# Kernel tuning notes

Measured on AMD Instinct MI355X. Metric: run time of the kernel, lower is better.

## Reference

```python
import jax, jax.numpy as jnp
import numpy as np

Z, K, HID = 128, 256, 512  # z_size, key_size, hidden_size


def setup_inputs() -> dict:
    key = jax.random.key(0)
    ks = jax.random.split(key, 12)
    B, T, Hi, Wi, Y = 512, 32, 32, 32, 4
    D = Hi * Wi
    s = 0.02
    f32 = jnp.float32
    return {
        "x_seq": jax.random.normal(ks[0], (B, T, Hi, Wi), f32),
        "W_enc": jax.random.normal(ks[1], (D, Z), f32) * s,
        "b_enc": jnp.zeros((Z,), f32),
        "W_lstm": jax.random.normal(ks[2], (K + 1, 4 * HID), f32) * s,
        "U_lstm": jax.random.normal(ks[3], (HID, 4 * HID), f32) * s,
        "b_lstm": jnp.zeros((4 * HID,), f32),
        "W_key": jax.random.normal(ks[4], (HID, K), f32) * s,
        "b_key": jnp.zeros((K,), f32),
        "W_g": jax.random.normal(ks[5], (HID, 1), f32) * s,
        "b_g": jnp.zeros((1,), f32),
        "W_y": jax.random.normal(ks[6], (HID, Y), f32) * s,
        "b_y": jnp.zeros((Y,), f32),
        "gamma": jnp.ones((Z,), f32),
        "beta": jnp.zeros((Z,), f32),
        "conf_gain": jnp.float32(1.0),
        "conf_bias": jnp.float32(0.0),
    }


def _forward(x_seq, W_enc, b_enc, W_lstm, U_lstm, b_lstm, W_key, b_key,
             W_g, b_g, W_y, b_y, gamma, beta, conf_gain, conf_bias):
    B, T = x_seq.shape[0], x_seq.shape[1]
    N = T + 1  # memory slots after final null step
    x = x_seq.reshape(B, T, -1)
    z = jax.nn.relu(x @ W_enc + b_enc)  # (B,T,Z) encoder stand-in
    # Faithful to TF source: list of (B,Z) stacks to (T,B,Z) and reduce axis 1
    # -> normalization is over the BATCH axis.
    mu = jnp.mean(z, axis=0, keepdims=True)
    var = jnp.var(z, axis=0, keepdims=True)
    z = (z - mu) / jnp.sqrt(var + 1e-8) * gamma + beta
    z_full = jnp.concatenate([z, jnp.zeros((B, 1, Z), z.dtype)], axis=1)  # (B,N,Z)

    def lstm_cell(x_in, h_in, c_in):
        gates = x_in @ W_lstm + h_in @ U_lstm + b_lstm
        i, f, g_, o = jnp.split(gates, 4, axis=-1)  # keras gate order i,f,c,o
        c_new = jax.nn.sigmoid(f) * c_in + jax.nn.sigmoid(i) * jnp.tanh(g_)
        h_new = jax.nn.sigmoid(o) * jnp.tanh(c_new)
        return h_new, c_new

    slot_ids = jnp.arange(N)

    def step(carry, inp):
        h, c, key_r, M_k, M_v = carry
        z_t, t = inp  # z_t: (B,Z), t: scalar step index
        # Faithful: source passes initial_state=(cell_state, hidden), swapping roles.
        h_new, c_new = lstm_cell(key_r, c, h)
        key_w = jax.nn.relu(h_new @ W_key + b_key)          # (B,K)
        g = jax.nn.sigmoid(h_new @ W_g + b_g)               # (B,1)
        y_lin = jax.nn.softmax(h_new @ W_y + b_y, axis=-1)  # (B,Y)
        # content-addressable read over the t filled slots
        sim = jnp.einsum('bz,bnz->bn', z_t, M_v)            # (B,N)
        mask = (slot_ids < t)[None, :]
        w_k = jax.nn.softmax(jnp.where(mask, sim, -1e9), axis=1)
        c_k = jax.nn.sigmoid(sim * conf_gain + conf_bias)   # (B,N)
        mem = jnp.concatenate([M_k, c_k[..., None]], axis=2)  # (B,N,K+1)
        weighted = jnp.einsum('bn,bnp->bp', w_k, mem)       # (B,K+1)
        key_r_new = jnp.where(t == 0, jnp.zeros_like(key_r), g * weighted)
        # write into slot t (pre-allocated memory, masked read above)
        M_k = M_k.at[:, t, :].set(key_w)
        M_v = M_v.at[:, t, :].set(z_t)
        return (h_new, c_new, key_r_new, M_k, M_v), y_lin

    h0 = jnp.zeros((B, HID), z.dtype)
    c0 = jnp.zeros((B, HID), z.dtype)
    kr0 = jnp.zeros((B, K + 1), z.dtype)
    Mk0 = jnp.zeros((B, N, K), z.dtype)
    Mv0 = jnp.zeros((B, N, Z), z.dtype)
    xs = (jnp.swapaxes(z_full, 0, 1), slot_ids)
    _, ys = jax.lax.scan(step, (h0, c0, kr0, Mk0, Mv0), xs)
    return ys[-1]  # y_pred_linear from the final (null-input) step


def reference(x_seq, W_enc, b_enc, W_lstm, U_lstm, b_lstm, W_key, b_key,
              W_g, b_g, W_y, b_y, gamma, beta, conf_gain, conf_bias):
    return _forward(x_seq, W_enc, b_enc, W_lstm, U_lstm, b_lstm, W_key, b_key,
                    W_g, b_g, W_y, b_y, gamma, beta, conf_gain, conf_bias)
```

## Files before the change

kernel.cpp:

```cpp
#include <hip/hip_runtime.h>

typedef __attribute__((ext_vector_type(8))) short short8;
typedef __attribute__((ext_vector_type(4))) float f32x4;
typedef __attribute__((ext_vector_type(8))) unsigned short ushort8;
typedef __attribute__((ext_vector_type(4))) unsigned short ushort4v;

__device__ __forceinline__ unsigned short f2bf(float f) {
  union { float f; unsigned u; } v; v.f = f;
  unsigned u = v.u;
  u += 0x7fffu + ((u >> 16) & 1u);
  return (unsigned short)(u >> 16);
}
__device__ __forceinline__ float sigm(float x) { return 1.f / (1.f + __expf(-x)); }
__device__ __forceinline__ float ftanh(float x) { return 1.f - 2.f / (__expf(2.f * x) + 1.f); }

__device__ __forceinline__ void gl16(const unsigned short* g, unsigned short* l) {
  __builtin_amdgcn_global_load_lds((const __attribute__((address_space(1))) void*)g,
                                   (__attribute__((address_space(3))) void*)l, 16, 0, 0);
}

__device__ __forceinline__ uint4 ld16_sys(const void* base, int off) {
  uint4 r;
  asm volatile("global_load_dwordx4 %0, %1, %2 sc0 sc1"
               : "=v"(r) : "v"(off), "s"(base) : "memory");
  return r;
}
__device__ __forceinline__ uint4 ld16_asm(const void* base, int off) {
  uint4 r;
  asm volatile("global_load_dwordx4 %0, %1, %2"
               : "=v"(r) : "v"(off), "s"(base) : "memory");
  return r;
}
__device__ __forceinline__ float ldf_sys(const void* base, int off) {
  float r;
  asm volatile("global_load_dword %0, %1, %2 sc0 sc1"
               : "=v"(r) : "v"(off), "s"(base) : "memory");
  return r;
}
__device__ __forceinline__ void stf_sys(void* base, int off, float v) {
  asm volatile("global_store_dword %0, %1, %2 sc0 sc1"
               :: "v"(off), "v"(v), "s"(base) : "memory");
}
__device__ __forceinline__ void sth_sys(void* base, int off, unsigned short v) {
  asm volatile("global_store_short %0, %1, %2 sc0 sc1"
               :: "v"(off), "v"(v), "s"(base) : "memory");
}
#define WAITVM(N)                                          \
  asm volatile("s_waitcnt vmcnt(" #N ")" ::: "memory");    \
  __builtin_amdgcn_sched_barrier(0)

__device__ __forceinline__ void gbar(unsigned* cnt, unsigned* gen) {
  asm volatile("s_waitcnt vmcnt(0)" ::: "memory");
  __syncthreads();
  if (threadIdx.x == 0) {
    unsigned g = __hip_atomic_load(gen, __ATOMIC_RELAXED, __HIP_MEMORY_SCOPE_AGENT);
    unsigned a = __hip_atomic_fetch_add(cnt, 1u, __ATOMIC_RELAXED, __HIP_MEMORY_SCOPE_AGENT);
    if (a == 255u) {
      __hip_atomic_store(cnt, 0u, __ATOMIC_RELAXED, __HIP_MEMORY_SCOPE_AGENT);
      __hip_atomic_store(gen, g + 1u, __ATOMIC_RELAXED, __HIP_MEMORY_SCOPE_AGENT);
    } else {
      while (__hip_atomic_load(gen, __ATOMIC_RELAXED, __HIP_MEMORY_SCOPE_AGENT) == g)
        __builtin_amdgcn_s_sleep(2);
    }
  }
  __syncthreads();
}

#define LSTR 40

__global__ void k_prep(const float* __restrict__ W_lstm, const float* __restrict__ U_lstm,
                       const float* __restrict__ W_enc, const float* __restrict__ W_key,
                       const float* __restrict__ W_g, const float* __restrict__ W_y,
                       const float* __restrict__ b_key, const float* __restrict__ b_g,
                       const float* __restrict__ b_y,
                       unsigned short* __restrict__ WcombT, unsigned short* __restrict__ Wk2T,
                       unsigned short* __restrict__ WencT, float* __restrict__ bias2,
                       unsigned short* __restrict__ xinA, unsigned short* __restrict__ xinB,
                       float* __restrict__ h, float* __restrict__ z_full,
                       unsigned* __restrict__ bar) {
  const int N1 = 2048 * 800, N2 = 320 * 512, N3 = 128 * 1024, N4 = 320,
            N5 = 512 * 800, N7 = 512 * 512, N8 = 512 * 128, N9 = 256;
  int i = blockIdx.x * 256 + threadIdx.x;
  if (i < N1) {
    int np = i / 800, k = i - np * 800;
    int j = np >> 2, gate = np & 3, n = gate * 512 + j;
    float v = 0.f;
    if (k < 257) v = W_lstm[k * 2048 + n];
    else if (k >= 288) v = U_lstm[(k - 288) * 2048 + n];
    WcombT[i] = f2bf(v);
    return;
  }
  i -= N1;
  if (i < N2) {
    int n = i / 512, k = i - n * 512;
    float v = 0.f;
    if (n < 256) v = W_key[k * 256 + n];
    else if (n == 256) v = W_g[k];
    else if (n < 261) v = W_y[k * 4 + (n - 257)];
    Wk2T[i] = f2bf(v);
    return;
  }
  i -= N2;
  if (i < N3) {
    int n = i / 1024, k = i - n * 1024;
    WencT[i] = f2bf(W_enc[k * 128 + n]);
    return;
  }
  i -= N3;
  if (i < N4) {
    float v = (i < 256) ? b_key[i] : (i == 256 ? b_g[0] : (i < 261 ? b_y[i - 257] : 0.f));
    bias2[i] = v;
    return;
  }
  i -= N4;
  if (i < N5) { xinA[i] = 0; return; }
  i -= N5;
  if (i < N5) { xinB[i] = 0; return; }
  i -= N5;
  if (i < N7) { h[i] = 0.f; return; }
  i -= N7;
  if (i < N8) {
    int b = i >> 7, z = i & 127;
    z_full[(b * 33 + 32) * 128 + z] = 0.f;
    return;
  }
  i -= N8;
  if (i < N9) bar[i] = 0;
}

__global__ __launch_bounds__(512) void k_enc(const float* __restrict__ x,
                                             const unsigned short* __restrict__ WencT,
                                             const float* __restrict__ b_enc,
                                             float* __restrict__ zbuf) {
  __shared__ __align__(16) unsigned short As[2][64 * LSTR];
  __shared__ __align__(16) unsigned short Bs[2][128 * LSTR];
  int tid = threadIdx.x;
  int m0 = blockIdx.x * 64;
  int lane = tid & 63, wid = tid >> 6;
  int wm = (wid >> 2) * 32, wn = (wid & 3) * 32;
  int q = lane >> 4, r = lane & 15;
  int ldrowA = tid >> 3, ldcA = (tid & 7) * 4;
  int ldrowB = tid >> 2, ldcB = (tid & 3) * 8;
  const float4* Ag = reinterpret_cast<const float4*>(x + (size_t)(m0 + ldrowA) * 1024);
  const uint4* Bg = reinterpret_cast<const uint4*>(WencT + (size_t)ldrowB * 1024);
  float4 ra = Ag[ldcA >> 2];
  uint4 rb = Bg[ldcB >> 3];
  f32x4 acc[2][2] = {};
  int s = 0;
  {
    ushort4v t4;
    t4[0] = f2bf(ra.x); t4[1] = f2bf(ra.y); t4[2] = f2bf(ra.z); t4[3] = f2bf(ra.w);
    *reinterpret_cast<ushort4v*>(&As[0][ldrowA * LSTR + ldcA]) = t4;
    *reinterpret_cast<uint4*>(&Bs[0][ldrowB * LSTR + ldcB]) = rb;
  }
  __syncthreads();
  for (int kk = 0; kk < 32; ++kk) {
    if (kk < 31) {
      int k0 = (kk + 1) * 32;
      ra = Ag[(k0 + ldcA) >> 2];
      rb = Bg[(k0 + ldcB) >> 3];
    }
    short8 a0 = *reinterpret_cast<const short8*>(&As[s][(wm + r) * LSTR + q * 8]);
    short8 a1 = *reinterpret_cast<const short8*>(&As[s][(wm + 16 + r) * LSTR + q * 8]);
    short8 b0 = *reinterpret_cast<const short8*>(&Bs[s][(wn + r) * LSTR + q * 8]);
    short8 b1 = *reinterpret_cast<const short8*>(&Bs[s][(wn + 16 + r) * LSTR + q * 8]);
    acc[0][0] = __builtin_amdgcn_mfma_f32_16x16x32_bf16(a0, b0, acc[0][0], 0, 0, 0);
    acc[0][1] = __builtin_amdgcn_mfma_f32_16x16x32_bf16(a0, b1, acc[0][1], 0, 0, 0);
    acc[1][0] = __builtin_amdgcn_mfma_f32_16x16x32_bf16(a1, b0, acc[1][0], 0, 0, 0);
    acc[1][1] = __builtin_amdgcn_mfma_f32_16x16x32_bf16(a1, b1, acc[1][1], 0, 0, 0);
    if (kk < 31) {
      ushort4v t4;
      t4[0] = f2bf(ra.x); t4[1] = f2bf(ra.y); t4[2] = f2bf(ra.z); t4[3] = f2bf(ra.w);
      *reinterpret_cast<ushort4v*>(&As[s ^ 1][ldrowA * LSTR + ldcA]) = t4;
      *reinterpret_cast<uint4*>(&Bs[s ^ 1][ldrowB * LSTR + ldcB]) = rb;
      s ^= 1;
    }
    __syncthreads();
  }
#pragma unroll
  for (int mt = 0; mt < 2; ++mt)
#pragma unroll
    for (int nt = 0; nt < 2; ++nt)
#pragma unroll
      for (int e = 0; e < 4; ++e) {
        int row = m0 + wm + mt * 16 + q * 4 + e;
        int col = wn + nt * 16 + r;
        zbuf[(size_t)row * 128 + col] = fmaxf(acc[mt][nt][e] + b_enc[col], 0.f);
      }
}

__global__ __launch_bounds__(256) void k_ln(const float* __restrict__ zbuf,
                                            const float* __restrict__ gamma,
                                            const float* __restrict__ beta,
                                            float* __restrict__ z_full) {
  int bid = blockIdx.x;
  int tstep = bid >> 3;
  int z0 = (bid & 7) * 16;
  int tid = threadIdx.x;
  int zl = tid & 15, bg = tid >> 4;
  __shared__ float ps[256], qs[256];
  __shared__ float muS[16], rsS[16];
  float s = 0.f, ss = 0.f;
  for (int ii = 0; ii < 32; ++ii) {
    int b = bg * 32 + ii;
    float v = zbuf[(size_t)(b * 32 + tstep) * 128 + z0 + zl];
    s += v; ss += v * v;
  }
  ps[tid] = s; qs[tid] = ss;
  __syncthreads();
  if (tid < 16) {
    float S = 0.f, Q = 0.f;
    for (int g2 = 0; g2 < 16; ++g2) { S += ps[g2 * 16 + tid]; Q += qs[g2 * 16 + tid]; }
    float mu = S / 512.f;
    float var = Q / 512.f - mu * mu;
    muS[tid] = mu;
    rsS[tid] = rsqrtf(var + 1e-8f);
  }
  __syncthreads();
  float ga = gamma[z0 + zl], be = beta[z0 + zl];
  float mu = muS[zl], rs = rsS[zl];
  for (int ii = 0; ii < 32; ++ii) {
    int b = bg * 32 + ii;
    float v = zbuf[(size_t)(b * 32 + tstep) * 128 + z0 + zl];
    z_full[(size_t)(b * 33 + tstep) * 128 + z0 + zl] = (v - mu) * rs * ga + be;
  }
}

__global__ __launch_bounds__(256) void k_attnpre(const float* __restrict__ z_full,
                                                 const float* __restrict__ cgain,
                                                 const float* __restrict__ cbias,
                                                 float* __restrict__ wk_tbl,
                                                 float* __restrict__ wck_tbl) {
  __shared__ float zs[33 * 128];
  __shared__ float sim[33 * 33];
  int b = blockIdx.x, tid = threadIdx.x;
  const float* zb = z_full + (size_t)b * 33 * 128;
  for (int i = tid; i < 33 * 128; i += 256) zs[i] = zb[i];
  __syncthreads();
  for (int p = tid; p < 33 * 33; p += 256) {
    int t = p / 33, n = p - t * 33;
    float s = 0.f;
    if (n < t) {
#pragma unroll 8
      for (int k2 = 0; k2 < 128; ++k2) s += zs[t * 128 + k2] * zs[n * 128 + k2];
    }
    sim[p] = s;
  }
  __syncthreads();
  if (tid >= 1 && tid < 33) {
    int t = tid;
    float cg = cgain[0], cb2 = cbias[0];
    float m = -3.0e38f;
    for (int n = 0; n < t; ++n) m = fmaxf(m, sim[t * 33 + n]);
    float ssum = 0.f;
    for (int n = 0; n < t; ++n) ssum += __expf(sim[t * 33 + n] - m);
    float inv = 1.f / ssum;
    float wck = 0.f;
    for (int n = 0; n < t; ++n) {
      float wk = __expf(sim[t * 33 + n] - m) * inv;
      wk_tbl[((size_t)b * 33 + t) * 33 + n] = wk;
      float ck = 1.f / (1.f + __expf(-(sim[t * 33 + n] * cg + cb2)));
      wck += wk * ck;
    }
    wck_tbl[b * 33 + t] = wck;
  }
}

__global__ __launch_bounds__(256) void k_loop(
    unsigned short* __restrict__ xinA, unsigned short* __restrict__ xinB,
    const unsigned short* __restrict__ WT, const float* __restrict__ b_lstm,
    float* __restrict__ h, unsigned short* __restrict__ hbf,
    const unsigned short* __restrict__ Wk2T, const float* __restrict__ bias2,
    float* __restrict__ Mk, float* __restrict__ logits,
    const float* __restrict__ Wg, const float* __restrict__ bg,
    const float* __restrict__ wk_tbl, const float* __restrict__ wck_tbl,
    float* __restrict__ out, unsigned* __restrict__ bar) {
  __shared__ __align__(16) unsigned short Bres[64 * 808];
  __shared__ __align__(16) unsigned char scr[43136];
  unsigned* cnt = bar;
  unsigned* gen = bar + 64;
  const int tid = threadIdx.x, bid = blockIdx.x;
  const int lane = tid & 63, w = tid >> 6;
  const int q = lane >> 4, r = lane & 15;
  const int wm = (w >> 1) * 32, wn = (w & 1) * 32;
  const int nn = bid & 31, mi = bid >> 5;
  const int m0 = mi * 64, n0g = nn * 64;

  for (int l = 0; l < 26; ++l) {
    int gw = l * 256 + w * 64;
    if (gw < 6464) {
      int g = gw + lane;
      int row = g / 101, cg = g - row * 101;
      int col = (cg >= 100) ? 792 : cg * 8;
      gl16(WT + (size_t)(n0g + row) * 800 + col, Bres + gw * 8);
    }
  }

  int srow[5], scol[5];
#pragma unroll
  for (int l = 0; l < 5; ++l) {
    int idx = l * 256 + tid;
    srow[l] = idx / 20;
    scol[l] = (idx - srow[l] * 20) * 8;
  }
  unsigned short* A0 = (unsigned short*)scr;
  unsigned short* A1 = (unsigned short*)(scr + 21504);

  const int jl = tid & 15, jg = nn * 16 + jl, rl0 = tid >> 4;
  const float bL0 = b_lstm[jg], bL1 = b_lstm[512 + jg],
              bL2 = b_lstm[1024 + jg], bL3 = b_lstm[1536 + jg];
  float hreg[4] = {0.f, 0.f, 0.f, 0.f};

  const int mi2 = bid / 5, ni2 = bid - mi2 * 5;

  asm volatile("s_waitcnt vmcnt(0)" ::: "memory");
  __syncthreads();

  for (int t = 0; t < 33; ++t) {
    const unsigned short* cur = (t & 1) ? xinB : xinA;
    unsigned short* nxt = (t & 1) ? xinA : xinB;

    uint4 R[5];
#pragma unroll
    for (int l = 0; l < 5; ++l)
      R[l] = ld16_sys(cur, ((m0 + srow[l]) * 800 + scol[l]) * 2);
    asm volatile("s_waitcnt vmcnt(0)" ::: "memory");
    __builtin_amdgcn_sched_barrier(0);
#pragma unroll
    for (int l = 0; l < 5; ++l)
      *(uint4*)&A0[srow[l] * 168 + scol[l]] = R[l];
    __syncthreads();

    f32x4 acc[2][2] = {};
    for (int c = 0; c < 5; ++c) {
      const unsigned short* Ac = (c & 1) ? A1 : A0;
      unsigned short* An = (c & 1) ? A0 : A1;
      if (c < 4) {
#pragma unroll
        for (int l = 0; l < 5; ++l)
          R[l] = ld16_sys(cur, ((m0 + srow[l]) * 800 + (c + 1) * 160 + scol[l]) * 2);
      }
#pragma unroll
      for (int ks = 0; ks < 5; ++ks) {
        short8 a0 = *(const short8*)&Ac[(wm + r) * 168 + ks * 32 + q * 8];
        short8 a1 = *(const short8*)&Ac[(wm + 16 + r) * 168 + ks * 32 + q * 8];
        short8 b0 = *(const short8*)&Bres[(wn + r) * 808 + c * 160 + ks * 32 + q * 8];
        short8 b1 = *(const short8*)&Bres[(wn + 16 + r) * 808 + c * 160 + ks * 32 + q * 8];
        acc[0][0] = __builtin_amdgcn_mfma_f32_16x16x32_bf16(a0, b0, acc[0][0], 0, 0, 0);
        acc[0][1] = __builtin_amdgcn_mfma_f32_16x16x32_bf16(a0, b1, acc[0][1], 0, 0, 0);
        acc[1][0] = __builtin_amdgcn_mfma_f32_16x16x32_bf16(a1, b0, acc[1][0], 0, 0, 0);
        acc[1][1] = __builtin_amdgcn_mfma_f32_16x16x32_bf16(a1, b1, acc[1][1], 0, 0, 0);
      }
      if (c < 4) {
        asm volatile("s_waitcnt vmcnt(0)" ::: "memory");
        __builtin_amdgcn_sched_barrier(0);
#pragma unroll
        for (int l = 0; l < 5; ++l)
          *(uint4*)&An[srow[l] * 168 + scol[l]] = R[l];
        __syncthreads();
      }
    }
    __syncthreads();

    float* Cs = (float*)scr;
#pragma unroll
    for (int mt = 0; mt < 2; ++mt)
#pragma unroll
      for (int nt = 0; nt < 2; ++nt)
#pragma unroll
        for (int e = 0; e < 4; ++e)
          Cs[(wm + mt * 16 + q * 4 + e) * 65 + wn + nt * 16 + r] = acc[mt][nt][e];
    __syncthreads();
#pragma unroll
    for (int it = 0; it < 4; ++it) {
      int rl = it * 16 + rl0;
      int brow = m0 + rl;
      float gi = Cs[rl * 65 + jl * 4 + 0] + bL0;
      float gf = Cs[rl * 65 + jl * 4 + 1] + bL1;
      float gc = Cs[rl * 65 + jl * 4 + 2] + bL2;
      float go = Cs[rl * 65 + jl * 4 + 3] + bL3;
      float cnew = sigm(gf) * hreg[it] + sigm(gi) * ftanh(gc);
      float hnew = sigm(go) * ftanh(cnew);
      hreg[it] = hnew;
      stf_sys(h, (brow * 512 + jg) * 4, hnew);
      sth_sys(hbf, (brow * 512 + jg) * 2, f2bf(hnew));
      sth_sys(nxt, (brow * 800 + 288 + jg) * 2, f2bf(cnew));
    }
    gbar(cnt, gen);

    if (bid < 40) {
      int m0b = mi2 * 64, n0b = ni2 * 64;
      int aoff0 = ((m0b + wm + r) * 512 + q * 8) * 2;
      int aoff1 = aoff0 + 16 * 1024;
      int boff0 = ((n0b + wn + r) * 512 + q * 8) * 2;
      int boff1 = boff0 + 16 * 1024;
      uint4 ab[4][2], bb[4][2];
      f32x4 acc2[2][2] = {};
#pragma unroll
      for (int j = 0; j < 3; ++j) {
        ab[j][0] = ld16_sys(hbf, aoff0 + j * 64);
        ab[j][1] = ld16_sys(hbf, aoff1 + j * 64);
        bb[j][0] = ld16_asm(Wk2T, boff0 + j * 64);
        bb[j][1] = ld16_asm(Wk2T, boff1 + j * 64);
      }
#pragma unroll
      for (int kk = 0; kk < 16; ++kk) {
        if (kk < 13) {
          int j = kk + 3;
          ab[j & 3][0] = ld16_sys(hbf, aoff0 + j * 64);
          ab[j & 3][1] = ld16_sys(hbf, aoff1 + j * 64);
          bb[j & 3][0] = ld16_asm(Wk2T, boff0 + j * 64);
          bb[j & 3][1] = ld16_asm(Wk2T, boff1 + j * 64);
        }
        if (kk < 13) { WAITVM(12); }
        else if (kk == 13) { WAITVM(8); }
        else if (kk == 14) { WAITVM(4); }
        else { WAITVM(0); }
        short8 a0 = *(const short8*)&ab[kk & 3][0];
        short8 a1 = *(const short8*)&ab[kk & 3][1];
        short8 b0s = *(const short8*)&bb[kk & 3][0];
        short8 b1s = *(const short8*)&bb[kk & 3][1];
        acc2[0][0] = __builtin_amdgcn_mfma_f32_16x16x32_bf16(a0, b0s, acc2[0][0], 0, 0, 0);
        acc2[0][1] = __builtin_amdgcn_mfma_f32_16x16x32_bf16(a0, b1s, acc2[0][1], 0, 0, 0);
        acc2[1][0] = __builtin_amdgcn_mfma_f32_16x16x32_bf16(a1, b0s, acc2[1][0], 0, 0, 0);
        acc2[1][1] = __builtin_amdgcn_mfma_f32_16x16x32_bf16(a1, b1s, acc2[1][1], 0, 0, 0);
      }
#pragma unroll
      for (int mt = 0; mt < 2; ++mt)
#pragma unroll
        for (int nt = 0; nt < 2; ++nt)
#pragma unroll
          for (int e2 = 0; e2 < 4; ++e2) {
            int row = m0b + wm + mt * 16 + q * 4 + e2;
            int np = n0b + wn + nt * 16 + r;
            float v = acc2[mt][nt][e2] + bias2[np];
            if (np < 256)
              stf_sys(Mk, ((row * 33 + t) * 256 + np) * 4, fmaxf(v, 0.f));
            else if (np >= 257 && np < 261)
              stf_sys(logits, (row * 4 + (np - 257)) * 4, v);
          }
    } else if (t > 0 && t < 32) {
      float* wkS = (float*)scr;
      float* red4 = (float*)(scr + 512);
      int b0 = bid - 40, b1 = b0 + 216, b2 = b0 + 432;
      bool v2 = (b2 < 512);
      int b2s = v2 ? b2 : b0;
      float hv[3][2];
      hv[0][0] = ldf_sys(h, (b0 * 512 + tid) * 4);
      hv[0][1] = ldf_sys(h, (b0 * 512 + 256 + tid) * 4);
      hv[1][0] = ldf_sys(h, (b1 * 512 + tid) * 4);
      hv[1][1] = ldf_sys(h, (b1 * 512 + 256 + tid) * 4);
      hv[2][0] = ldf_sys(h, (b2s * 512 + tid) * 4);
      hv[2][1] = ldf_sys(h, (b2s * 512 + 256 + tid) * 4);
      asm volatile("s_waitcnt vmcnt(0)" ::: "memory");
      __builtin_amdgcn_sched_barrier(0);
      float wg0 = Wg[tid], wg1 = Wg[256 + tid], bgv = bg[0];
#pragma unroll
      for (int rr = 0; rr < 3; ++rr) {
        int b = (rr == 0) ? b0 : (rr == 1) ? b1 : b2s;
        bool wr = (rr < 2) || v2;
        float sd = hv[rr][0] * wg0 + hv[rr][1] * wg1;
#pragma unroll
        for (int off = 32; off > 0; off >>= 1) sd += __shfl_down(sd, off);
        if (lane == 0) red4[w] = sd;
        if (tid < t) wkS[tid] = wk_tbl[((size_t)b * 33 + t) * 33 + tid];
        __syncthreads();
        float g = 1.f / (1.f + __expf(-(red4[0] + red4[1] + red4[2] + red4[3] + bgv)));
        float p0 = 0.f, p1 = 0.f, p2 = 0.f, p3 = 0.f;
        int n = 0;
        for (; n + 4 <= t; n += 4) {
          p0 += wkS[n] * Mk[((size_t)b * 33 + n) * 256 + tid];
          p1 += wkS[n + 1] * Mk[((size_t)b * 33 + n + 1) * 256 + tid];
          p2 += wkS[n + 2] * Mk[((size_t)b * 33 + n + 2) * 256 + tid];
          p3 += wkS[n + 3] * Mk[((size_t)b * 33 + n + 3) * 256 + tid];
        }
        for (; n < t; ++n) p0 += wkS[n] * Mk[((size_t)b * 33 + n) * 256 + tid];
        if (wr) {
          sth_sys(nxt, (b * 800 + tid) * 2, f2bf(g * ((p0 + p1) + (p2 + p3))));
          if (tid == 0) sth_sys(nxt, (b * 800 + 256) * 2, f2bf(g * wck_tbl[b * 33 + t]));
        }
        __syncthreads();
      }
    }
    gbar(cnt, gen);
  }
  if (bid == 0) {
    for (int r2 = tid; r2 < 512; r2 += 256) {
      float a = logits[r2 * 4], b2 = logits[r2 * 4 + 1],
            c2 = logits[r2 * 4 + 2], d2 = logits[r2 * 4 + 3];
      float m = fmaxf(fmaxf(a, b2), fmaxf(c2, d2));
      float ea = __expf(a - m), eb = __expf(b2 - m), ec = __expf(c2 - m), ed = __expf(d2 - m);
      float ssum = ea + eb + ec + ed;
      out[r2 * 4] = ea / ssum; out[r2 * 4 + 1] = eb / ssum;
      out[r2 * 4 + 2] = ec / ssum; out[r2 * 4 + 3] = ed / ssum;
    }
  }
}

__global__ __launch_bounds__(256) void k_gates(const unsigned short* __restrict__ xin,
                                               const unsigned short* __restrict__ WT,
                                               const float* __restrict__ b_lstm,
                                               float* __restrict__ h,
                                               unsigned short* __restrict__ hbf,
                                               unsigned short* __restrict__ xin_nxt) {
  __shared__ __align__(16) unsigned short As[2][64 * LSTR];
  __shared__ __align__(16) unsigned short Bs[2][64 * LSTR];
  __shared__ float Cs[64 * 65];
  int tid = threadIdx.x;
  int nn = blockIdx.x;
  int m0 = blockIdx.y * 64;
  int n0 = nn * 64;
  int lane = tid & 63, wid = tid >> 6;
  int wm = (wid >> 1) * 32, wn = (wid & 1) * 32;
  int q = lane >> 4, r = lane & 15;
  int ldrow = tid >> 2, ldc = (tid & 3) * 8;
  const uint4* Ag = reinterpret_cast<const uint4*>(xin + (size_t)(m0 + ldrow) * 800);
  const uint4* Bg = reinterpret_cast<const uint4*>(WT + (size_t)(n0 + ldrow) * 800);
  uint4 ra = Ag[ldc >> 3], rb = Bg[ldc >> 3];
  f32x4 acc[2][2] = {};
  int s = 0;
  *reinterpret_cast<uint4*>(&As[0][ldrow * LSTR + ldc]) = ra;
  *reinterpret_cast<uint4*>(&Bs[0][ldrow * LSTR + ldc]) = rb;
  __syncthreads();
  for (int kk = 0; kk < 25; ++kk) {
    if (kk < 24) {
      int k0 = (kk + 1) * 32;
      ra = Ag[(k0 + ldc) >> 3];
      rb = Bg[(k0 + ldc) >> 3];
    }
    short8 a0 = *reinterpret_cast<const short8*>(&As[s][(wm + r) * LSTR + q * 8]);
    short8 a1 = *reinterpret_cast<const short8*>(&As[s][(wm + 16 + r) * LSTR + q * 8]);
    short8 b0 = *reinterpret_cast<const short8*>(&Bs[s][(wn + r) * LSTR + q * 8]);
    short8 b1 = *reinterpret_cast<const short8*>(&Bs[s][(wn + 16 + r) * LSTR + q * 8]);
    acc[0][0] = __builtin_amdgcn_mfma_f32_16x16x32_bf16(a0, b0, acc[0][0], 0, 0, 0);
    acc[0][1] = __builtin_amdgcn_mfma_f32_16x16x32_bf16(a0, b1, acc[0][1], 0, 0, 0);
    acc[1][0] = __builtin_amdgcn_mfma_f32_16x16x32_bf16(a1, b0, acc[1][0], 0, 0, 0);
    acc[1][1] = __builtin_amdgcn_mfma_f32_16x16x32_bf16(a1, b1, acc[1][1], 0, 0, 0);
    if (kk < 24) {
      *reinterpret_cast<uint4*>(&As[s ^ 1][ldrow * LSTR + ldc]) = ra;
      *reinterpret_cast<uint4*>(&Bs[s ^ 1][ldrow * LSTR + ldc]) = rb;
      s ^= 1;
    }
    __syncthreads();
  }
#pragma unroll
  for (int mt = 0; mt < 2; ++mt)
#pragma unroll
    for (int nt = 0; nt < 2; ++nt)
#pragma unroll
      for (int e = 0; e < 4; ++e)
        Cs[(wm + mt * 16 + q * 4 + e) * 65 + wn + nt * 16 + r] = acc[mt][nt][e];
  __syncthreads();
#pragma unroll
  for (int it = 0; it < 4; ++it) {
    int id = it * 256 + tid;
    int rl = id >> 4, jl = id & 15;
    int brow = m0 + rl;
    int j = nn * 16 + jl;
    float gi = Cs[rl * 65 + jl * 4 + 0] + b_lstm[j];
    float gf = Cs[rl * 65 + jl * 4 + 1] + b_lstm[512 + j];
    float gg = Cs[rl * 65 + jl * 4 + 2] + b_lstm[1024 + j];
    float go = Cs[rl * 65 + jl * 4 + 3] + b_lstm[1536 + j];
    float hold = h[brow * 512 + j];
    float cnew = sigm(gf) * hold + sigm(gi) * ftanh(gg);
    float hnew = sigm(go) * ftanh(cnew);
    h[brow * 512 + j] = hnew;
    hbf[brow * 512 + j] = f2bf(hnew);
    xin_nxt[brow * 800 + 288 + j] = f2bf(cnew);
  }
}

__global__ __launch_bounds__(256) void k_head(const unsigned short* __restrict__ hbf,
                                              const unsigned short* __restrict__ Wk2T,
                                              const float* __restrict__ bias2,
                                              float* __restrict__ Mk,
                                              float* __restrict__ logits,
                                              const float* __restrict__ h,
                                              const float* __restrict__ Wg,
                                              const float* __restrict__ bg,
                                              const float* __restrict__ wk_tbl,
                                              const float* __restrict__ wck_tbl,
                                              unsigned short* __restrict__ xin_nxt,
                                              int t) {
  __shared__ __align__(16) unsigned short As[2][64 * LSTR];
  __shared__ __align__(16) unsigned short Bs[2][64 * LSTR];
  __shared__ float wkS[33];
  __shared__ float red[256];
  int bid = blockIdx.x;
  int tid = threadIdx.x;
  if (bid < 40) {
    int mi = bid / 5, ni = bid - mi * 5;
    int m0 = mi * 64, n0 = ni * 64;
    int lane = tid & 63, wid = tid >> 6;
    int wm = (wid >> 1) * 32, wn = (wid & 1) * 32;
    int q = lane >> 4, r = lane & 15;
    int ldrow = tid >> 2, ldc = (tid & 3) * 8;
    const uint4* Ag = reinterpret_cast<const uint4*>(hbf + (size_t)(m0 + ldrow) * 512);
    const uint4* Bg = reinterpret_cast<const uint4*>(Wk2T + (size_t)(n0 + ldrow) * 512);
    uint4 ra = Ag[ldc >> 3], rb = Bg[ldc >> 3];
    f32x4 acc[2][2] = {};
    int s = 0;
    *reinterpret_cast<uint4*>(&As[0][ldrow * LSTR + ldc]) = ra;
    *reinterpret_cast<uint4*>(&Bs[0][ldrow * LSTR + ldc]) = rb;
    __syncthreads();
    for (int kk = 0; kk < 16; ++kk) {
      if (kk < 15) {
        int k0 = (kk + 1) * 32;
        ra = Ag[(k0 + ldc) >> 3];
        rb = Bg[(k0 + ldc) >> 3];
      }
      short8 a0 = *reinterpret_cast<const short8*>(&As[s][(wm + r) * LSTR + q * 8]);
      short8 a1 = *reinterpret_cast<const short8*>(&As[s][(wm + 16 + r) * LSTR + q * 8]);
      short8 b0 = *reinterpret_cast<const short8*>(&Bs[s][(wn + r) * LSTR + q * 8]);
      short8 b1 = *reinterpret_cast<const short8*>(&Bs[s][(wn + 16 + r) * LSTR + q * 8]);
      acc[0][0] = __builtin_amdgcn_mfma_f32_16x16x32_bf16(a0, b0, acc[0][0], 0, 0, 0);
      acc[0][1] = __builtin_amdgcn_mfma_f32_16x16x32_bf16(a0, b1, acc[0][1], 0, 0, 0);
      acc[1][0] = __builtin_amdgcn_mfma_f32_16x16x32_bf16(a1, b0, acc[1][0], 0, 0, 0);
      acc[1][1] = __builtin_amdgcn_mfma_f32_16x16x32_bf16(a1, b1, acc[1][1], 0, 0, 0);
      if (kk < 15) {
        *reinterpret_cast<uint4*>(&As[s ^ 1][ldrow * LSTR + ldc]) = ra;
        *reinterpret_cast<uint4*>(&Bs[s ^ 1][ldrow * LSTR + ldc]) = rb;
        s ^= 1;
      }
      __syncthreads();
    }
#pragma unroll
    for (int mt = 0; mt < 2; ++mt)
#pragma unroll
      for (int nt = 0; nt < 2; ++nt)
#pragma unroll
        for (int e = 0; e < 4; ++e) {
          int row = m0 + wm + mt * 16 + q * 4 + e;
          int np = n0 + wn + nt * 16 + r;
          float v = acc[mt][nt][e] + bias2[np];
          if (np < 256) Mk[(size_t)(row * 33 + t) * 256 + np] = fmaxf(v, 0.f);
          else if (np >= 257 && np < 261) logits[row * 4 + (np - 257)] = v;
        }
  } else {
    if (t == 0 || t == 32) return;
    int b = bid - 40;
    float s = h[b * 512 + tid] * Wg[tid] + h[b * 512 + 256 + tid] * Wg[256 + tid];
    red[tid] = s;
    if (tid < t) wkS[tid] = wk_tbl[((size_t)b * 33 + t) * 33 + tid];
    __syncthreads();
    for (int off = 128; off > 0; off >>= 1) {
      if (tid < off) red[tid] += red[tid + off];
      __syncthreads();
    }
    float g = 1.f / (1.f + __expf(-(red[0] + bg[0])));
    float acc = 0.f;
    for (int n = 0; n < t; ++n) acc += wkS[n] * Mk[((size_t)b * 33 + n) * 256 + tid];
    xin_nxt[b * 800 + tid] = f2bf(g * acc);
    if (tid == 0) xin_nxt[b * 800 + 256] = f2bf(g * wck_tbl[b * 33 + t]);
  }
}

__global__ void k_softmax(const float* __restrict__ logits, float* __restrict__ out) {
  int tid = threadIdx.x;
  for (int r2 = tid; r2 < 512; r2 += 256) {
    float a = logits[r2 * 4], b = logits[r2 * 4 + 1], c = logits[r2 * 4 + 2], d = logits[r2 * 4 + 3];
    float m = fmaxf(fmaxf(a, b), fmaxf(c, d));
    float ea = __expf(a - m), eb = __expf(b - m), ec = __expf(c - m), ed = __expf(d - m);
    float s = ea + eb + ec + ed;
    out[r2 * 4] = ea / s; out[r2 * 4 + 1] = eb / s;
    out[r2 * 4 + 2] = ec / s; out[r2 * 4 + 3] = ed / s;
  }
}

extern "C" void kernel_launch(void* const* d_in, const int* in_sizes, int n_in,
                              void* d_out, int out_size, void* d_ws, size_t ws_size,
                              hipStream_t stream) {
  const float* x_seq = (const float*)d_in[0];
  const float* W_enc = (const float*)d_in[1];
  const float* b_enc = (const float*)d_in[2];
  const float* W_lstm = (const float*)d_in[3];
  const float* U_lstm = (const float*)d_in[4];
  const float* b_lstm = (const float*)d_in[5];
  const float* W_key = (const float*)d_in[6];
  const float* b_key = (const float*)d_in[7];
  const float* W_g = (const float*)d_in[8];
  const float* b_g = (const float*)d_in[9];
  const float* W_y = (const float*)d_in[10];
  const float* b_y = (const float*)d_in[11];
  const float* gamma = (const float*)d_in[12];
  const float* beta = (const float*)d_in[13];
  const float* cg_ = (const float*)d_in[14];
  const float* cb = (const float*)d_in[15];

  char* p = (char*)d_ws;
  auto alloc = [&](size_t bytes) {
    char* r = p;
    p += (bytes + 255) & ~(size_t)255;
    return r;
  };
  float* zbuf = (float*)alloc((size_t)16384 * 128 * 4);
  float* z_full = (float*)alloc((size_t)512 * 33 * 128 * 4);
  unsigned short* WcombT = (unsigned short*)alloc((size_t)2048 * 800 * 2);
  unsigned short* WencT = (unsigned short*)alloc((size_t)128 * 1024 * 2);
  unsigned short* Wk2T = (unsigned short*)alloc((size_t)320 * 512 * 2);
  float* bias2 = (float*)alloc(320 * 4);
  unsigned short* xinA = (unsigned short*)alloc((size_t)512 * 800 * 2);
  unsigned short* xinB = (unsigned short*)alloc((size_t)512 * 800 * 2);
  float* h = (float*)alloc((size_t)512 * 512 * 4);
  unsigned short* hbf = (unsigned short*)alloc((size_t)512 * 512 * 2);
  float* Mk = (float*)alloc((size_t)512 * 33 * 256 * 4);
  float* logits = (float*)alloc((size_t)512 * 4 * 4);
  float* wk_tbl = (float*)alloc((size_t)512 * 33 * 33 * 4);
  float* wck_tbl = (float*)alloc((size_t)512 * 33 * 4);
  unsigned* bar = (unsigned*)alloc(1024);
  float* outp = (float*)d_out;

  const int prep_total = 2048 * 800 + 320 * 512 + 128 * 1024 + 320 + 2 * 512 * 800 +
                         512 * 512 + 512 * 128 + 256;
  k_prep<<<(prep_total + 255) / 256, 256, 0, stream>>>(
      W_lstm, U_lstm, W_enc, W_key, W_g, W_y, b_key, b_g, b_y,
      WcombT, Wk2T, WencT, bias2, xinA, xinB, h, z_full, bar);
  k_enc<<<256, 512, 0, stream>>>(x_seq, WencT, b_enc, zbuf);
  k_ln<<<256, 256, 0, stream>>>(zbuf, gamma, beta, z_full);
  k_attnpre<<<512, 256, 0, stream>>>(z_full, cg_, cb, wk_tbl, wck_tbl);

  void* cargs[16];
  cargs[0] = &xinA;  cargs[1] = &xinB;   cargs[2] = &WcombT; cargs[3] = &b_lstm;
  cargs[4] = &h;     cargs[5] = &hbf;    cargs[6] = &Wk2T;   cargs[7] = &bias2;
  cargs[8] = &Mk;    cargs[9] = &logits; cargs[10] = &W_g;   cargs[11] = &b_g;
  cargs[12] = &wk_tbl; cargs[13] = &wck_tbl; cargs[14] = &outp; cargs[15] = &bar;
  hipError_t ce = hipLaunchCooperativeKernel((const void*)k_loop, dim3(256), dim3(256),
                                             cargs, 0u, stream);
  if (ce != hipSuccess) {
    for (int t = 0; t < 33; ++t) {
      unsigned short* cur = (t & 1) ? xinB : xinA;
      unsigned short* nxt = (t & 1) ? xinA : xinB;
      k_gates<<<dim3(32, 8), 256, 0, stream>>>(cur, WcombT, b_lstm, h, hbf, nxt);
      k_head<<<552, 256, 0, stream>>>(hbf, Wk2T, bias2, Mk, logits, h,
                                      W_g, b_g, wk_tbl, wck_tbl, nxt, t);
    }
    k_softmax<<<1, 256, 0, stream>>>(logits, outp);
  }
}
```

Measured before the change: 840.9 us.

## Replace atomic-counter grid barrier with per-block flag barrier

Replaces the centralized atomic fetch-add grid barrier with a per-block flag array. Each block writes its generation to its own padded slot, and each thread polls one block's flag with uncached loads. This removes serialized atomics on one counter and the single-thread spin from the per-step sync. The attention-read stage is also restructured to load h per row inside the loop rather than prefetching three rows. The flag buffer grows to 16 KB, and the final logits read now uses system-coherent loads.

```diff
diff --git a/kernel.cpp b/kernel.cpp
--- a/kernel.cpp
+++ b/kernel.cpp
@@ -37,10 +37,20 @@
                : "=v"(r) : "v"(off), "s"(base) : "memory");
   return r;
 }
+__device__ __forceinline__ unsigned ldu_sys(const void* base, int off) {
+  unsigned r;
+  asm volatile("global_load_dword %0, %1, %2 sc0 sc1"
+               : "=v"(r) : "v"(off), "s"(base) : "memory");
+  return r;
+}
 __device__ __forceinline__ void stf_sys(void* base, int off, float v) {
   asm volatile("global_store_dword %0, %1, %2 sc0 sc1"
                :: "v"(off), "v"(v), "s"(base) : "memory");
 }
+__device__ __forceinline__ void stu_sys(void* base, int off, unsigned v) {
+  asm volatile("global_store_dword %0, %1, %2 sc0 sc1"
+               :: "v"(off), "v"(v), "s"(base) : "memory");
+}
 __device__ __forceinline__ void sth_sys(void* base, int off, unsigned short v) {
   asm volatile("global_store_short %0, %1, %2 sc0 sc1"
                :: "v"(off), "v"(v), "s"(base) : "memory");
@@ -49,19 +59,16 @@
   asm volatile("s_waitcnt vmcnt(" #N ")" ::: "memory");    \
   __builtin_amdgcn_sched_barrier(0)
 
-__device__ __forceinline__ void gbar(unsigned* cnt, unsigned* gen) {
+__device__ __forceinline__ void gbar(unsigned* flags, unsigned gen) {
   asm volatile("s_waitcnt vmcnt(0)" ::: "memory");
   __syncthreads();
-  if (threadIdx.x == 0) {
-    unsigned g = __hip_atomic_load(gen, __ATOMIC_RELAXED, __HIP_MEMORY_SCOPE_AGENT);
-    unsigned a = __hip_atomic_fetch_add(cnt, 1u, __ATOMIC_RELAXED, __HIP_MEMORY_SCOPE_AGENT);
-    if (a == 255u) {
-      __hip_atomic_store(cnt, 0u, __ATOMIC_RELAXED, __HIP_MEMORY_SCOPE_AGENT);
-      __hip_atomic_store(gen, g + 1u, __ATOMIC_RELAXED, __HIP_MEMORY_SCOPE_AGENT);
-    } else {
-      while (__hip_atomic_load(gen, __ATOMIC_RELAXED, __HIP_MEMORY_SCOPE_AGENT) == g)
-        __builtin_amdgcn_s_sleep(2);
-    }
+  if (threadIdx.x == 0) stu_sys(flags, (int)(blockIdx.x * 64), gen);
+  int off = (int)(threadIdx.x * 64);
+  for (;;) {
+    unsigned v = ldu_sys(flags, off);
+    asm volatile("s_waitcnt vmcnt(0)" ::: "memory");
+    if (v >= gen) break;
+    __builtin_amdgcn_s_sleep(1);
   }
   __syncthreads();
 }
@@ -79,7 +86,7 @@
                        float* __restrict__ h, float* __restrict__ z_full,
                        unsigned* __restrict__ bar) {
   const int N1 = 2048 * 800, N2 = 320 * 512, N3 = 128 * 1024, N4 = 320,
-            N5 = 512 * 800, N7 = 512 * 512, N8 = 512 * 128, N9 = 256;
+            N5 = 512 * 800, N7 = 512 * 512, N8 = 512 * 128, N9 = 4096;
   int i = blockIdx.x * 256 + threadIdx.x;
   if (i < N1) {
     int np = i / 800, k = i - np * 800;
@@ -277,14 +284,13 @@
     float* __restrict__ out, unsigned* __restrict__ bar) {
   __shared__ __align__(16) unsigned short Bres[64 * 808];
   __shared__ __align__(16) unsigned char scr[43136];
-  unsigned* cnt = bar;
-  unsigned* gen = bar + 64;
   const int tid = threadIdx.x, bid = blockIdx.x;
   const int lane = tid & 63, w = tid >> 6;
   const int q = lane >> 4, r = lane & 15;
   const int wm = (w >> 1) * 32, wn = (w & 1) * 32;
   const int nn = bid & 31, mi = bid >> 5;
   const int m0 = mi * 64, n0g = nn * 64;
+  unsigned gen = 0;
 
   for (int l = 0; l < 26; ++l) {
     int gw = l * 256 + w * 64;
@@ -386,7 +392,7 @@
       sth_sys(hbf, (brow * 512 + jg) * 2, f2bf(hnew));
       sth_sys(nxt, (brow * 800 + 288 + jg) * 2, f2bf(cnew));
     }
-    gbar(cnt, gen);
+    ++gen; gbar(bar, gen);
 
     if (bid < 40) {
       int m0b = mi2 * 64, n0b = ni2 * 64;
@@ -442,52 +448,43 @@
     } else if (t > 0 && t < 32) {
       float* wkS = (float*)scr;
       float* red4 = (float*)(scr + 512);
-      int b0 = bid - 40, b1 = b0 + 216, b2 = b0 + 432;
-      bool v2 = (b2 < 512);
-      int b2s = v2 ? b2 : b0;
-      float hv[3][2];
-      hv[0][0] = ldf_sys(h, (b0 * 512 + tid) * 4);
-      hv[0][1] = ldf_sys(h, (b0 * 512 + 256 + tid) * 4);
-      hv[1][0] = ldf_sys(h, (b1 * 512 + tid) * 4);
-      hv[1][1] = ldf_sys(h, (b1 * 512 + 256 + tid) * 4);
-      hv[2][0] = ldf_sys(h, (b2s * 512 + tid) * 4);
-      hv[2][1] = ldf_sys(h, (b2s * 512 + 256 + tid) * 4);
-      asm volatile("s_waitcnt vmcnt(0)" ::: "memory");
-      __builtin_amdgcn_sched_barrier(0);
-      float wg0 = Wg[tid], wg1 = Wg[256 + tid], bgv = bg[0];
-#pragma unroll
       for (int rr = 0; rr < 3; ++rr) {
-        int b = (rr == 0) ? b0 : (rr == 1) ? b1 : b2s;
-        bool wr = (rr < 2) || v2;
-        float sd = hv[rr][0] * wg0 + hv[rr][1] * wg1;
-#pragma unroll
-        for (int off = 32; off > 0; off >>= 1) sd += __shfl_down(sd, off);
-        if (lane == 0) red4[w] = sd;
-        if (tid < t) wkS[tid] = wk_tbl[((size_t)b * 33 + t) * 33 + tid];
-        __syncthreads();
-        float g = 1.f / (1.f + __expf(-(red4[0] + red4[1] + red4[2] + red4[3] + bgv)));
-        float p0 = 0.f, p1 = 0.f, p2 = 0.f, p3 = 0.f;
-        int n = 0;
-        for (; n + 4 <= t; n += 4) {
-          p0 += wkS[n] * Mk[((size_t)b * 33 + n) * 256 + tid];
-          p1 += wkS[n + 1] * Mk[((size_t)b * 33 + n + 1) * 256 + tid];
-          p2 += wkS[n + 2] * Mk[((size_t)b * 33 + n + 2) * 256 + tid];
-          p3 += wkS[n + 3] * Mk[((size_t)b * 33 + n + 3) * 256 + tid];
-        }
-        for (; n < t; ++n) p0 += wkS[n] * Mk[((size_t)b * 33 + n) * 256 + tid];
-        if (wr) {
+        int b = (bid - 40) + 216 * rr;
+        if (b < 512) {
+          float ha = ldf_sys(h, (b * 512 + tid) * 4);
+          float hb = ldf_sys(h, (b * 512 + 256 + tid) * 4);
+          asm volatile("s_waitcnt vmcnt(0)" ::: "memory");
+          float sd = ha * Wg[tid] + hb * Wg[256 + tid];
+#pragma unroll
+          for (int off = 32; off > 0; off >>= 1) sd += __shfl_down(sd, off);
+          if (lane == 0) red4[w] = sd;
+          if (tid < t) wkS[tid] = wk_tbl[((size_t)b * 33 + t) * 33 + tid];
+          __syncthreads();
+          float g = 1.f / (1.f + __expf(-(red4[0] + red4[1] + red4[2] + red4[3] + bg[0])));
+          float p0 = 0.f, p1 = 0.f, p2 = 0.f, p3 = 0.f;
+          int n = 0;
+          for (; n + 4 <= t; n += 4) {
+            p0 += wkS[n] * Mk[((size_t)b * 33 + n) * 256 + tid];
+            p1 += wkS[n + 1] * Mk[((size_t)b * 33 + n + 1) * 256 + tid];
+            p2 += wkS[n + 2] * Mk[((size_t)b * 33 + n + 2) * 256 + tid];
+            p3 += wkS[n + 3] * Mk[((size_t)b * 33 + n + 3) * 256 + tid];
+          }
+          for (; n < t; ++n) p0 += wkS[n] * Mk[((size_t)b * 33 + n) * 256 + tid];
           sth_sys(nxt, (b * 800 + tid) * 2, f2bf(g * ((p0 + p1) + (p2 + p3))));
           if (tid == 0) sth_sys(nxt, (b * 800 + 256) * 2, f2bf(g * wck_tbl[b * 33 + t]));
+          __syncthreads();
         }
-        __syncthreads();
-      }
-    }
-    gbar(cnt, gen);
+      }
+    }
+    ++gen; gbar(bar, gen);
   }
   if (bid == 0) {
     for (int r2 = tid; r2 < 512; r2 += 256) {
-      float a = logits[r2 * 4], b2 = logits[r2 * 4 + 1],
-            c2 = logits[r2 * 4 + 2], d2 = logits[r2 * 4 + 3];
+      float a = ldf_sys(logits, r2 * 16);
+      float b2 = ldf_sys(logits, r2 * 16 + 4);
+      float c2 = ldf_sys(logits, r2 * 16 + 8);
+      float d2 = ldf_sys(logits, r2 * 16 + 12);
+      asm volatile("s_waitcnt vmcnt(0)" ::: "memory");
       float m = fmaxf(fmaxf(a, b2), fmaxf(c2, d2));
       float ea = __expf(a - m), eb = __expf(b2 - m), ec = __expf(c2 - m), ed = __expf(d2 - m);
       float ssum = ea + eb + ec + ed;
@@ -707,11 +704,11 @@
   float* logits = (float*)alloc((size_t)512 * 4 * 4);
   float* wk_tbl = (float*)alloc((size_t)512 * 33 * 33 * 4);
   float* wck_tbl = (float*)alloc((size_t)512 * 33 * 4);
-  unsigned* bar = (unsigned*)alloc(1024);
+  unsigned* bar = (unsigned*)alloc(16384);
   float* outp = (float*)d_out;
 
   const int prep_total = 2048 * 800 + 320 * 512 + 128 * 1024 + 320 + 2 * 512 * 800 +
-                         512 * 512 + 512 * 128 + 256;
+                         512 * 512 + 512 * 128 + 4096;
   k_prep<<<(prep_total + 255) / 256, 256, 0, stream>>>(
       W_lstm, U_lstm, W_enc, W_key, W_g, W_y, b_key, b_g, b_y,
       WcombT, Wk2T, WencT, bias2, xinA, xinB, h, z_full, bar);
```

Measured after the change: 782.7 us. -6.9%, faster.
